# Performance work log

Measured on AMD Instinct MI355X. Metric: run time of the kernel, lower is better.

The kernel has to match this reference:

```python
import jax, jax.numpy as jnp
import numpy as np

NUM_HEADS = 8
EPS = 1e-6


def conv1x1(x, w, b):
    # x: [b,c,h,w], w: [out,in], b: [out]  (torch Conv2d 1x1 weight squeezed)
    return jnp.einsum('bchw,oc->bohw', x, w) + b[None, :, None, None]


def feature_map(x):
    return jax.nn.elu(x) + 1.0


def setup_inputs() -> dict:
    key = jax.random.key(0)
    ks = jax.random.split(key, 9)
    C = 512
    s = 1.0 / np.sqrt(C)
    x = jax.random.normal(ks[0], (8, C, 64, 64), dtype=jnp.float32)
    wq = jax.random.normal(ks[1], (C, C), dtype=jnp.float32) * s
    wk = jax.random.normal(ks[2], (C, C), dtype=jnp.float32) * s
    wv = jax.random.normal(ks[3], (C, C), dtype=jnp.float32) * s
    wo = jax.random.normal(ks[4], (C, C), dtype=jnp.float32) * s
    bq = jax.random.normal(ks[5], (C,), dtype=jnp.float32) * 0.01
    bk = jax.random.normal(ks[6], (C,), dtype=jnp.float32) * 0.01
    bv = jax.random.normal(ks[7], (C,), dtype=jnp.float32) * 0.01
    bo = jax.random.normal(ks[8], (C,), dtype=jnp.float32) * 0.01
    return {'x': x, 'wq': wq, 'bq': bq, 'wk': wk, 'bk': bk,
            'wv': wv, 'bv': bv, 'wo': wo, 'bo': bo}


def reference(x, wq, bq, wk, bk, wv, bv, wo, bo):
    b, c, h, w = x.shape
    nh = NUM_HEADS
    hd = c // nh
    L = h * w

    def to_heads(t):
        # [b,c,h,w] -> [b,nh,L,hd]
        return t.reshape(b, nh, hd, L).transpose(0, 1, 3, 2)

    Q = feature_map(to_heads(conv1x1(x, wq, bq)))
    K = feature_map(to_heads(conv1x1(x, wk, bk)))
    V = to_heads(conv1x1(x, wv, bv)) / L  # values / v_length

    KV = jnp.einsum('bhld,bhlv->bhdv', K, V)                 # [b,nh,hd,hd]
    Z = 1.0 / (jnp.einsum('bhld,bhd->bhl', Q, K.sum(axis=-2)) + EPS)
    out = jnp.einsum('bhld,bhdv,bhl->bhlv', Q, KV, Z) * L    # [b,nh,L,hd]

    out = out.transpose(0, 1, 3, 2).reshape(b, c, h, w)
    return conv1x1(out, wo, bo)
```

## Files before the change

### kernel.cpp

```cpp
#include <hip/hip_runtime.h>
#include <hip/hip_bf16.h>
#include <stdint.h>

#define BATCH 8
#define CCH   512
#define NHD   8
#define HD    64
#define LLEN  4096
#define M1    1536

typedef __bf16 bf16x8 __attribute__((ext_vector_type(8)));
typedef __bf16 bf16x4 __attribute__((ext_vector_type(4)));
typedef float  f32x4  __attribute__((ext_vector_type(4)));

__device__ __forceinline__ f32x4 mfma16(bf16x8 a, bf16x8 b, f32x4 c) {
  return __builtin_amdgcn_mfma_f32_16x16x32_bf16(a, b, c, 0, 0, 0);
}

__device__ __forceinline__ void gload_lds16(const void* g, void* l) {
  __builtin_amdgcn_global_load_lds(
      (const __attribute__((address_space(1))) uint32_t*)(uintptr_t)g,
      (__attribute__((address_space(3))) uint32_t*)(uintptr_t)l,
      16, 0, 0);
}

__global__ void pack_w(const float* __restrict__ wq, const float* __restrict__ wk,
                       const float* __restrict__ wv, const float* __restrict__ wo,
                       const float* __restrict__ bq, const float* __restrict__ bk,
                       const float* __restrict__ bv,
                       __bf16* __restrict__ wqkvb, __bf16* __restrict__ wob,
                       float* __restrict__ biasq) {
  const int n = M1 * CCH + CCH * CCH + M1;
  for (int i = blockIdx.x * blockDim.x + threadIdx.x; i < n; i += gridDim.x * blockDim.x) {
    if (i < M1 * CCH) {
      int r = i >> 9, c = i & 511;
      float v = (r < 512) ? wq[r * 512 + c]
              : (r < 1024) ? wk[(r - 512) * 512 + c]
                           : wv[(r - 1024) * 512 + c];
      wqkvb[i] = (__bf16)v;
    } else if (i < M1 * CCH + CCH * CCH) {
      int j = i - M1 * CCH;
      wob[j] = (__bf16)wo[j];
    } else {
      int j = i - M1 * CCH - CCH * CCH;
      biasq[j] = (j < 512) ? bq[j] : (j < 1024) ? bk[j - 512] : bv[j - 1024];
    }
  }
}

__global__ __launch_bounds__(256) void transpose_x(const float* __restrict__ x,
                                                   __bf16* __restrict__ xt) {
  __shared__ float tile[64][65];
  const int b = blockIdx.z, c0 = blockIdx.y * 64, l0 = blockIdx.x * 64;
  const int t = threadIdx.x;
  const int lq = (t & 15) * 4, cr = t >> 4;
  const float* xp = x + ((size_t)b * CCH + c0) * LLEN + l0;
#pragma unroll
  for (int q = 0; q < 4; ++q) {
    const int c = cr + q * 16;
    float4 v = *(const float4*)(xp + (size_t)c * LLEN + lq);
    tile[c][lq + 0] = v.x;
    tile[c][lq + 1] = v.y;
    tile[c][lq + 2] = v.z;
    tile[c][lq + 3] = v.w;
  }
  __syncthreads();
  __bf16* xo = xt + ((size_t)b * LLEN + l0) * CCH + c0;
  const int c4 = (t & 15) * 4, lr = t >> 4;
#pragma unroll
  for (int p = 0; p < 4; ++p) {
    const int l = lr + p * 16;
    bf16x4 o;
#pragma unroll
    for (int i = 0; i < 4; ++i) o[i] = (__bf16)tile[c4 + i][l];
    *(bf16x4*)(xo + (size_t)l * CCH + c4) = o;
  }
}

template <int EPI>
__global__ __launch_bounds__(256) void gemm_k(
    const __bf16* __restrict__ A, const __bf16* __restrict__ Bm,
    const float* __restrict__ bias,
    __bf16* __restrict__ qt, __bf16* __restrict__ kcm, __bf16* __restrict__ vcm,
    float* __restrict__ out) {
  __shared__ __attribute__((aligned(16))) __bf16 As[128 * 32];
  __shared__ __attribute__((aligned(16))) __bf16 Bs[128 * 32];
  const int b  = blockIdx.z;
  const int n0 = blockIdx.x * 128;
  const int m0 = blockIdx.y * 128;
  const int tid = threadIdx.x;
  const int ll = tid & 63, w = tid >> 6;
  const int wr = w >> 1, wc = w & 1;
  const int lhi = ll >> 4, llo = ll & 15;
  const int r4 = ll >> 2, c8e = (ll & 3) * 8;

  const __bf16* Ap = A + (size_t)m0 * CCH;
  const __bf16* Bp = Bm + ((size_t)b * LLEN + n0) * CCH;

  f32x4 acc[4][4];
#pragma unroll
  for (int i = 0; i < 4; ++i)
#pragma unroll
    for (int j = 0; j < 4; ++j) acc[i][j] = (f32x4){0.f, 0.f, 0.f, 0.f};

  for (int kt = 0; kt < 16; ++kt) {
    const int k0 = kt * 32;
    if (kt) __syncthreads();
#pragma unroll
    for (int i = 0; i < 2; ++i) {
      const int rb = i * 64 + w * 16;
      gload_lds16(Ap + (size_t)(rb + r4) * CCH + k0 + c8e, As + rb * 32);
      gload_lds16(Bp + (size_t)(rb + r4) * CCH + k0 + c8e, Bs + rb * 32);
    }
    __syncthreads();
    bf16x8 af[4], bfr[4];
#pragma unroll
    for (int i = 0; i < 4; ++i) {
      af[i]  = *(const bf16x8*)(As + (wr * 64 + i * 16 + llo) * 32 + lhi * 8);
      bfr[i] = *(const bf16x8*)(Bs + (wc * 64 + i * 16 + llo) * 32 + lhi * 8);
    }
#pragma unroll
    for (int i = 0; i < 4; ++i)
#pragma unroll
      for (int j = 0; j < 4; ++j) acc[i][j] = mfma16(af[i], bfr[j], acc[i][j]);
  }

#pragma unroll
  for (int i = 0; i < 4; ++i) {
    const int o0 = m0 + wr * 64 + i * 16 + lhi * 4;
#pragma unroll
    for (int j = 0; j < 4; ++j) {
      const int col = n0 + wc * 64 + j * 16 + llo;
      if (EPI == 0) {
        if (m0 < 512) {
          bf16x4 pk;
#pragma unroll
          for (int r = 0; r < 4; ++r) {
            float t = acc[i][j][r] + bias[o0 + r];
            t = t > 0.f ? t + 1.f : __expf(t);
            pk[r] = (__bf16)t;
          }
          *(bf16x4*)(qt + ((size_t)b * LLEN + col) * CCH + o0) = pk;
        } else if (m0 < 1024) {
#pragma unroll
          for (int r = 0; r < 4; ++r) {
            float t = acc[i][j][r] + bias[o0 + r];
            t = t > 0.f ? t + 1.f : __expf(t);
            kcm[((size_t)b * CCH + (o0 - 512 + r)) * LLEN + col] = (__bf16)t;
          }
        } else {
#pragma unroll
          for (int r = 0; r < 4; ++r)
            vcm[((size_t)b * CCH + (o0 - 1024 + r)) * LLEN + col] =
                (__bf16)(acc[i][j][r] + bias[o0 + r]);
        }
      } else {
#pragma unroll
        for (int r = 0; r < 4; ++r)
          out[((size_t)b * CCH + o0 + r) * LLEN + col] = acc[i][j][r] + bias[o0 + r];
      }
    }
  }
}

__global__ __launch_bounds__(64) void kv_part_k(const __bf16* __restrict__ kcm,
                                                const __bf16* __restrict__ vcm,
                                                float* __restrict__ part,
                                                float* __restrict__ part_ks) {
  const int lc = blockIdx.x, bh = blockIdx.y;
  const int b = bh >> 3, h = bh & 7;
  const int ll = threadIdx.x, lhi = ll >> 4, llo = ll & 15;
  const __bf16* Kp = kcm + ((size_t)b * CCH + h * 64) * LLEN;
  const __bf16* Vp = vcm + ((size_t)b * CCH + h * 64) * LLEN;
  f32x4 acc[4][4];
#pragma unroll
  for (int i = 0; i < 4; ++i)
#pragma unroll
    for (int j = 0; j < 4; ++j) acc[i][j] = (f32x4){0.f, 0.f, 0.f, 0.f};
  float ks[4] = {0.f, 0.f, 0.f, 0.f};
  const int base = lc * 512 + lhi * 8;
  for (int kt = 0; kt < 16; ++kt) {
    const int k0 = base + kt * 32;
    bf16x8 af[4], bfr[4];
#pragma unroll
    for (int i = 0; i < 4; ++i) af[i]  = *(const bf16x8*)(Kp + (size_t)(i * 16 + llo) * LLEN + k0);
#pragma unroll
    for (int i = 0; i < 4; ++i) bfr[i] = *(const bf16x8*)(Vp + (size_t)(i * 16 + llo) * LLEN + k0);
#pragma unroll
    for (int i = 0; i < 4; ++i)
#pragma unroll
      for (int r = 0; r < 8; ++r) ks[i] += (float)af[i][r];
#pragma unroll
    for (int i = 0; i < 4; ++i)
#pragma unroll
      for (int j = 0; j < 4; ++j) acc[i][j] = mfma16(af[i], bfr[j], acc[i][j]);
  }
  float* op = part + ((size_t)lc * 64 + bh) * 4096;
#pragma unroll
  for (int i = 0; i < 4; ++i)
#pragma unroll
    for (int j = 0; j < 4; ++j)
#pragma unroll
      for (int r = 0; r < 4; ++r) {
        int d = i * 16 + lhi * 4 + r, v = j * 16 + llo;
        op[d * 64 + v] = acc[i][j][r];
      }
  float* pks = part_ks + ((size_t)lc * 64 + bh) * 64;
#pragma unroll
  for (int i = 0; i < 4; ++i) {
    float s = ks[i];
    s += __shfl_xor(s, 16);
    s += __shfl_xor(s, 32);
    if (lhi == 0) pks[i * 16 + llo] = s;
  }
}

__global__ void kv_red_k(const float* __restrict__ part, float* __restrict__ kv) {
  const int i = blockIdx.x * blockDim.x + threadIdx.x;
  float s = 0.f;
#pragma unroll
  for (int lc = 0; lc < 8; ++lc) s += part[(size_t)lc * 262144 + i];
  kv[i] = s;
}

__global__ void ksum_red_k(const float* __restrict__ part_ks, float* __restrict__ ksum) {
  const int i = blockIdx.x * blockDim.x + threadIdx.x;
  float s = 0.f;
#pragma unroll
  for (int lc = 0; lc < 8; ++lc) s += part_ks[(size_t)lc * 4096 + i];
  ksum[i] = s;
}

__global__ __launch_bounds__(256) void apply_k(const __bf16* __restrict__ qt,
                                               const float* __restrict__ kv,
                                               const float* __restrict__ ksum,
                                               __bf16* __restrict__ attn) {
  __shared__ __attribute__((aligned(16))) __bf16 kvT[64 * 68];
  __shared__ float zb[256];
  const int lc = blockIdx.x, bh = blockIdx.y;
  const int b = bh >> 3, h = bh & 7;
  const int tid = threadIdx.x;
  const float* kvp = kv + (size_t)bh * 4096;
  for (int i = tid; i < 4096; i += 256) {
    int d = i >> 6, v = i & 63;
    kvT[v * 68 + d] = (__bf16)kvp[i];
  }
  const int l = lc * 256 + tid;
  const __bf16* qp = qt + ((size_t)b * LLEN + l) * CCH + h * 64;
  const float* ksp = ksum + bh * 64;
  float s = 0.f;
#pragma unroll
  for (int d8 = 0; d8 < 64; d8 += 8) {
    bf16x8 qv = *(const bf16x8*)(qp + d8);
#pragma unroll
    for (int i = 0; i < 8; ++i) s += (float)qv[i] * ksp[d8 + i];
  }
  zb[tid] = 1.0f / (s + 1e-6f);
  __syncthreads();

  const int ll = tid & 63, w = tid >> 6, lhi = ll >> 4, llo = ll & 15;
  f32x4 acc[4][4];
#pragma unroll
  for (int i = 0; i < 4; ++i)
#pragma unroll
    for (int j = 0; j < 4; ++j) acc[i][j] = (f32x4){0.f, 0.f, 0.f, 0.f};
  const __bf16* qbase = qt + ((size_t)b * LLEN + lc * 256 + w * 64) * CCH + h * 64;
#pragma unroll
  for (int kt = 0; kt < 2; ++kt) {
    const int k8 = kt * 32 + lhi * 8;
    bf16x8 af[4], bfr[4];
#pragma unroll
    for (int i = 0; i < 4; ++i)
      af[i] = *(const bf16x8*)(qbase + (size_t)(i * 16 + llo) * CCH + k8);
#pragma unroll
    for (int j = 0; j < 4; ++j) {
      const __bf16* pb = kvT + (j * 16 + llo) * 68 + k8;
      ((bf16x4*)&bfr[j])[0] = *(const bf16x4*)pb;
      ((bf16x4*)&bfr[j])[1] = *(const bf16x4*)(pb + 4);
    }
#pragma unroll
    for (int i = 0; i < 4; ++i)
#pragma unroll
      for (int j = 0; j < 4; ++j) acc[i][j] = mfma16(af[i], bfr[j], acc[i][j]);
  }
  __bf16* ap = attn + ((size_t)b * LLEN + lc * 256) * CCH + h * 64;
#pragma unroll
  for (int i = 0; i < 4; ++i)
#pragma unroll
    for (int j = 0; j < 4; ++j)
#pragma unroll
      for (int r = 0; r < 4; ++r) {
        int ml = w * 64 + i * 16 + lhi * 4 + r;
        int v = j * 16 + llo;
        ap[(size_t)ml * CCH + v] = (__bf16)(acc[i][j][r] * zb[ml]);
      }
}

extern "C" void kernel_launch(void* const* d_in, const int* in_sizes, int n_in,
                              void* d_out, int out_size, void* d_ws, size_t ws_size,
                              hipStream_t stream) {
  const float* x  = (const float*)d_in[0];
  const float* wq = (const float*)d_in[1];
  const float* bq = (const float*)d_in[2];
  const float* wk = (const float*)d_in[3];
  const float* bk = (const float*)d_in[4];
  const float* wv = (const float*)d_in[5];
  const float* bv = (const float*)d_in[6];
  const float* wo = (const float*)d_in[7];
  const float* bo = (const float*)d_in[8];
  float* out = (float*)d_out;

  char* p = (char*)d_ws;
  __bf16* xt    = (__bf16*)p; p += (size_t)BATCH * LLEN * CCH * 2;
  __bf16* qt    = (__bf16*)p; p += (size_t)BATCH * LLEN * CCH * 2;
  __bf16* kcm   = (__bf16*)p; p += (size_t)BATCH * CCH * LLEN * 2;
  __bf16* vcm   = (__bf16*)p; p += (size_t)BATCH * CCH * LLEN * 2;
  __bf16* wqkvb = (__bf16*)p; p += (size_t)M1 * CCH * 2;
  __bf16* wob   = (__bf16*)p; p += (size_t)CCH * CCH * 2;
  float*  biasq = (float*)p;  p += (size_t)M1 * 4;
  float*  ksum  = (float*)p;  p += (size_t)BATCH * CCH * 4;
  float*  part  = (float*)p;  p += (size_t)8 * 64 * HD * HD * 4;
  float*  kvb   = (float*)p;  p += (size_t)64 * HD * HD * 4;
  float*  pks   = (float*)p;  p += (size_t)8 * 64 * 64 * 4;
  __bf16* attn  = xt;

  pack_w<<<1024, 256, 0, stream>>>(wq, wk, wv, wo, bq, bk, bv, wqkvb, wob, biasq);
  transpose_x<<<dim3(64, 8, BATCH), 256, 0, stream>>>(x, xt);
  gemm_k<0><<<dim3(32, 12, BATCH), 256, 0, stream>>>(wqkvb, xt, biasq, qt, kcm, vcm, nullptr);
  kv_part_k<<<dim3(8, 64), 64, 0, stream>>>(kcm, vcm, part, pks);
  kv_red_k<<<1024, 256, 0, stream>>>(part, kvb);
  ksum_red_k<<<16, 256, 0, stream>>>(pks, ksum);
  apply_k<<<dim3(16, 64), 256, 0, stream>>>(qt, kvb, ksum, attn);
  gemm_k<1><<<dim3(32, 4, BATCH), 256, 0, stream>>>(wob, attn, bo, nullptr, nullptr, nullptr, out);
}
```

Measured before the change: 172.9 us.

## Replace GEMM with 256x256-tile, triple-buffered, swizzled-LDS pipelined kernel

Replaces the 128x128 single-buffered GEMM with a 256x256 tile kernel using 512 threads and three LDS stages. Global-to-LDS loads for step t+2 are issued while MFMAs run on step t, and the LDS layout is XOR-swizzled to avoid bank conflicts. Priority raising around the MFMA blocks and split A-half staging interleave memory and math. The larger tile cuts global reloads of A and B but halves the number of blocks, which lowers grid parallelism and raises register and LDS pressure.

```diff
diff --git a/kernel.cpp b/kernel.cpp
--- a/kernel.cpp
+++ b/kernel.cpp
@@ -77,57 +77,108 @@
   }
 }
 
+#define STAGE_A(kt, base)                                                    \
+  {                                                                          \
+    _Pragma("unroll") for (int p = 0; p < 2; ++p)                            \
+        gload_lds16(Ag + (size_t)sR[p] * CCH + (kt) * 32 + sK[p],            \
+                    lds + (base) + sDst[p]);                                 \
+  }
+#define STAGE_B(kt, base)                                                    \
+  {                                                                          \
+    _Pragma("unroll") for (int p = 0; p < 2; ++p)                            \
+        gload_lds16(Bg + (size_t)sR[p] * CCH + (kt) * 32 + sK[p],            \
+                    lds + (base) + 8192 + sDst[p]);                          \
+  }
+
 template <int EPI>
-__global__ __launch_bounds__(256) void gemm_k(
+__global__ __launch_bounds__(512, 2) void gemm256(
     const __bf16* __restrict__ A, const __bf16* __restrict__ Bm,
     const float* __restrict__ bias,
     __bf16* __restrict__ qt, __bf16* __restrict__ kcm, __bf16* __restrict__ vcm,
     float* __restrict__ out) {
-  __shared__ __attribute__((aligned(16))) __bf16 As[128 * 32];
-  __shared__ __attribute__((aligned(16))) __bf16 Bs[128 * 32];
+  __shared__ __attribute__((aligned(16))) __bf16 lds[3 * 16384];
   const int b  = blockIdx.z;
-  const int n0 = blockIdx.x * 128;
-  const int m0 = blockIdx.y * 128;
+  const int n0 = blockIdx.x * 256;
+  const int m0 = blockIdx.y * 256;
   const int tid = threadIdx.x;
   const int ll = tid & 63, w = tid >> 6;
-  const int wr = w >> 1, wc = w & 1;
+  const int wr = w >> 2, wc = w & 3;
   const int lhi = ll >> 4, llo = ll & 15;
-  const int r4 = ll >> 2, c8e = (ll & 3) * 8;
-
-  const __bf16* Ap = A + (size_t)m0 * CCH;
-  const __bf16* Bp = Bm + ((size_t)b * LLEN + n0) * CCH;
-
-  f32x4 acc[4][4];
-#pragma unroll
-  for (int i = 0; i < 4; ++i)
-#pragma unroll
-    for (int j = 0; j < 4; ++j) acc[i][j] = (f32x4){0.f, 0.f, 0.f, 0.f};
-
-  for (int kt = 0; kt < 16; ++kt) {
-    const int k0 = kt * 32;
-    if (kt) __syncthreads();
-#pragma unroll
-    for (int i = 0; i < 2; ++i) {
-      const int rb = i * 64 + w * 16;
-      gload_lds16(Ap + (size_t)(rb + r4) * CCH + k0 + c8e, As + rb * 32);
-      gload_lds16(Bp + (size_t)(rb + r4) * CCH + k0 + c8e, Bs + rb * 32);
+
+  int aoff[8], boff[4];
+#pragma unroll
+  for (int m = 0; m < 8; ++m) {
+    int R = wr * 128 + m * 16 + llo;
+    aoff[m] = ((R >> 1) << 6) + (((((R & 1) << 2) | lhi) ^ ((R >> 1) & 7)) << 3);
+  }
+#pragma unroll
+  for (int n = 0; n < 4; ++n) {
+    int R = wc * 64 + n * 16 + llo;
+    boff[n] = ((R >> 1) << 6) + (((((R & 1) << 2) | lhi) ^ ((R >> 1) & 7)) << 3) + 8192;
+  }
+
+  int sR[2], sK[2], sDst[2];
+#pragma unroll
+  for (int p = 0; p < 2; ++p) {
+    int idx = p * 512 + tid;
+    int r2 = idx >> 3, c7u = (idx & 7) ^ (r2 & 7);
+    sR[p]   = (r2 << 1) | (c7u >> 2);
+    sK[p]   = (c7u & 3) << 3;
+    sDst[p] = idx * 8;
+  }
+  const __bf16* Ag = A + (size_t)m0 * CCH;
+  const __bf16* Bg = Bm + ((size_t)b * LLEN + n0) * CCH;
+
+  STAGE_A(0, 0) STAGE_B(0, 0)
+  STAGE_A(1, 16384) STAGE_B(1, 16384)
+  asm volatile("s_waitcnt vmcnt(4)" ::: "memory");
+  __builtin_amdgcn_s_barrier();
+
+  f32x4 acc[8][4] = {};
+  int bi = 0;
+  for (int t = 0; t < 16; ++t) {
+    const int abase = bi * 16384;
+    const int sb = ((bi == 0) ? 2 : bi - 1) * 16384;
+    bf16x8 af[4], bfr[4];
+#pragma unroll
+    for (int i = 0; i < 4; ++i) af[i] = *(const bf16x8*)(lds + abase + aoff[i]);
+#pragma unroll
+    for (int j = 0; j < 4; ++j) bfr[j] = *(const bf16x8*)(lds + abase + boff[j]);
+    if (t + 2 < 16) STAGE_A(t + 2, sb)
+    __builtin_amdgcn_s_barrier();
+    asm volatile("s_waitcnt lgkmcnt(0)" ::: "memory");
+    __builtin_amdgcn_sched_barrier(0);
+    __builtin_amdgcn_s_setprio(1);
+#pragma unroll
+    for (int i = 0; i < 4; ++i)
+#pragma unroll
+      for (int j = 0; j < 4; ++j) acc[i][j] = mfma16(af[i], bfr[j], acc[i][j]);
+    __builtin_amdgcn_s_setprio(0);
+    __builtin_amdgcn_s_barrier();
+#pragma unroll
+    for (int i = 0; i < 4; ++i) af[i] = *(const bf16x8*)(lds + abase + aoff[4 + i]);
+    if (t + 2 < 16) {
+      STAGE_B(t + 2, sb)
+      asm volatile("s_waitcnt vmcnt(4)" ::: "memory");
+    } else {
+      asm volatile("s_waitcnt vmcnt(0)" ::: "memory");
     }
-    __syncthreads();
-    bf16x8 af[4], bfr[4];
-#pragma unroll
-    for (int i = 0; i < 4; ++i) {
-      af[i]  = *(const bf16x8*)(As + (wr * 64 + i * 16 + llo) * 32 + lhi * 8);
-      bfr[i] = *(const bf16x8*)(Bs + (wc * 64 + i * 16 + llo) * 32 + lhi * 8);
-    }
-#pragma unroll
-    for (int i = 0; i < 4; ++i)
-#pragma unroll
-      for (int j = 0; j < 4; ++j) acc[i][j] = mfma16(af[i], bfr[j], acc[i][j]);
-  }
-
-#pragma unroll
-  for (int i = 0; i < 4; ++i) {
-    const int o0 = m0 + wr * 64 + i * 16 + lhi * 4;
+    __builtin_amdgcn_s_barrier();
+    asm volatile("s_waitcnt lgkmcnt(0)" ::: "memory");
+    __builtin_amdgcn_sched_barrier(0);
+    __builtin_amdgcn_s_setprio(1);
+#pragma unroll
+    for (int i = 0; i < 4; ++i)
+#pragma unroll
+      for (int j = 0; j < 4; ++j) acc[4 + i][j] = mfma16(af[i], bfr[j], acc[4 + i][j]);
+    __builtin_amdgcn_s_setprio(0);
+    __builtin_amdgcn_s_barrier();
+    bi = (bi == 2) ? 0 : bi + 1;
+  }
+
+#pragma unroll
+  for (int i = 0; i < 8; ++i) {
+    const int o0 = m0 + wr * 128 + i * 16 + lhi * 4;
 #pragma unroll
     for (int j = 0; j < 4; ++j) {
       const int col = n0 + wc * 64 + j * 16 + llo;
@@ -136,17 +187,17 @@
           bf16x4 pk;
 #pragma unroll
           for (int r = 0; r < 4; ++r) {
-            float t = acc[i][j][r] + bias[o0 + r];
-            t = t > 0.f ? t + 1.f : __expf(t);
-            pk[r] = (__bf16)t;
+            float tv = acc[i][j][r] + bias[o0 + r];
+            tv = tv > 0.f ? tv + 1.f : __expf(tv);
+            pk[r] = (__bf16)tv;
           }
           *(bf16x4*)(qt + ((size_t)b * LLEN + col) * CCH + o0) = pk;
         } else if (m0 < 1024) {
 #pragma unroll
           for (int r = 0; r < 4; ++r) {
-            float t = acc[i][j][r] + bias[o0 + r];
-            t = t > 0.f ? t + 1.f : __expf(t);
-            kcm[((size_t)b * CCH + (o0 - 512 + r)) * LLEN + col] = (__bf16)t;
+            float tv = acc[i][j][r] + bias[o0 + r];
+            tv = tv > 0.f ? tv + 1.f : __expf(tv);
+            kcm[((size_t)b * CCH + (o0 - 512 + r)) * LLEN + col] = (__bf16)tv;
           }
         } else {
 #pragma unroll
@@ -326,10 +377,10 @@
 
   pack_w<<<1024, 256, 0, stream>>>(wq, wk, wv, wo, bq, bk, bv, wqkvb, wob, biasq);
   transpose_x<<<dim3(64, 8, BATCH), 256, 0, stream>>>(x, xt);
-  gemm_k<0><<<dim3(32, 12, BATCH), 256, 0, stream>>>(wqkvb, xt, biasq, qt, kcm, vcm, nullptr);
+  gemm256<0><<<dim3(16, 6, BATCH), 512, 0, stream>>>(wqkvb, xt, biasq, qt, kcm, vcm, nullptr);
   kv_part_k<<<dim3(8, 64), 64, 0, stream>>>(kcm, vcm, part, pks);
   kv_red_k<<<1024, 256, 0, stream>>>(part, kvb);
   ksum_red_k<<<16, 256, 0, stream>>>(pks, ksum);
   apply_k<<<dim3(16, 64), 256, 0, stream>>>(qt, kvb, ksum, attn);
-  gemm_k<1><<<dim3(32, 4, BATCH), 256, 0, stream>>>(wob, attn, bo, nullptr, nullptr, nullptr, out);
-}
+  gemm256<1><<<dim3(16, 2, BATCH), 512, 0, stream>>>(wob, attn, bo, nullptr, nullptr, nullptr, out);
+}
```

New measurement: 170.2 us. No clear change (-1.6%).
